# Kernel optimization log

Hardware: AMD Instinct MI355X
Metric: run time of the kernel (lower is better)

The kernel has to match this reference:

```python
import jax, jax.numpy as jnp
import numpy as np

BN_EPS = 1e-5
LEAKY_SLOPE = 0.01
DK = 64


def setup_inputs() -> dict:
    key = jax.random.key(0)
    ks = jax.random.split(key, 9)
    B, N, C = 8, 2048, 256
    H, dk, dv = 8, 64, 64
    return {
        "x": jax.random.normal(ks[0], (B, N, C), jnp.float32),
        "Wq": jax.random.normal(ks[1], (H, dk, C), jnp.float32) * (1.0 / np.sqrt(C)),
        "Wk": jax.random.normal(ks[2], (H, dk, C), jnp.float32) * (1.0 / np.sqrt(C)),
        "Wv": jax.random.normal(ks[3], (H, dv, C), jnp.float32) * (1.0 / np.sqrt(C)),
        "Wp": jax.random.normal(ks[4], (C, H * dv), jnp.float32) * (1.0 / np.sqrt(H * dv)),
        "bn_gamma": jax.random.uniform(ks[5], (C,), jnp.float32, 0.5, 1.5),
        "bn_beta": jax.random.normal(ks[6], (C,), jnp.float32) * 0.1,
        "bn_mean": jax.random.normal(ks[7], (C,), jnp.float32) * 0.1,
        "bn_var": jax.random.uniform(ks[8], (C,), jnp.float32, 0.5, 1.5),
    }


def reference(x, Wq, Wk, Wv, Wp, bn_gamma, bn_beta, bn_mean, bn_var):
    # x: [B,N,C]; per-head 1x1 Conv1d projections batched over heads h.
    q = jnp.einsum("bnc,hkc->bhnk", x, Wq)   # [B,H,N,dk]
    k = jnp.einsum("bnc,hkc->bhnk", x, Wk)   # [B,H,N,dk]
    v = jnp.einsum("bnc,hvc->bhnv", x, Wv)   # [B,H,N,dv]
    energy = jnp.einsum("bhnk,bhmk->bhnm", q, k)  # [B,H,N,N]
    scale = 1.0 / jnp.sqrt(jnp.float32(DK))
    attn = jax.nn.softmax(energy * scale, axis=-1)
    xw = jnp.einsum("bhnm,bhmv->bhnv", attn, v)   # [B,H,N,dv]
    # torch.cat(heads, dim=2) -> [B,N,H*dv] with head-major ordering
    B, H, N, dv = xw.shape
    cat = jnp.transpose(xw, (0, 2, 1, 3)).reshape(B, N, H * dv)
    # LBRD: 1x1 conv (no bias) + BatchNorm1d (inference stats) + LeakyReLU + Dropout(0)
    y = jnp.einsum("bnf,cf->bnc", cat, Wp)
    y = (y - bn_mean) * (bn_gamma * jax.lax.rsqrt(bn_var + BN_EPS)) + bn_beta
    y = jnp.where(y >= 0, y, LEAKY_SLOPE * y)
    return y
```

## Files before the change

kernel.cpp:

```cpp
#include <hip/hip_runtime.h>
#include <hip/hip_bf16.h>

typedef unsigned short u16;
typedef unsigned int u32;
typedef float  f32x4 __attribute__((ext_vector_type(4)));
typedef short  s16x8 __attribute__((ext_vector_type(8)));

#define DEV static __device__ __forceinline__

DEV u16 f2bf(float f){ union{float f; unsigned int i;} c; c.f=f; unsigned int i=c.i;
                       return (u16)((i + 0x7FFFu + ((i>>16)&1u))>>16); }

DEV u32 pkbf(float a, float b){
  union{ __hip_bfloat162 h; u32 u; } c;
  c.h = __float22bfloat162_rn(make_float2(a, b));
  return c.u;
}

DEV float exp2a(float x){
#if __has_builtin(__builtin_amdgcn_exp2f)
  return __builtin_amdgcn_exp2f(x);
#else
  return exp2f(x);
#endif
}

DEV s16x8 ld_frag(const u16* p){
  union{ s16x8 v; uint2 u[2]; } r;
  r.u[0] = *(const uint2*)(p);
  r.u[1] = *(const uint2*)(p+16);
  return r.v;
}

__global__ __launch_bounds__(256) void cvt_kernel(const float* __restrict__ src,
                                                  u16* __restrict__ dst, int n4)
{
  int i = blockIdx.x*256 + threadIdx.x;
  if (i >= n4) return;
  float4 v = *(const float4*)(src + (size_t)i*4);
  ushort4 o;
  o.x = f2bf(v.x); o.y = f2bf(v.y); o.z = f2bf(v.z); o.w = f2bf(v.w);
  *(ushort4*)(dst + (size_t)i*4) = o;
}

__global__ __launch_bounds__(256) void kv_kernel(
    const u16* __restrict__ x, const u16* __restrict__ Wk,
    const u16* __restrict__ Wv, u16* __restrict__ kbuf, u16* __restrict__ vbuf)
{
  const int isV = blockIdx.z;
  const u16* W = isV ? Wv : Wk;
  const int m0 = blockIdx.x*64, j0 = blockIdx.y*64;
  __shared__ u16 at[64][40];
  __shared__ u16 bt[64][40];
  const int tid = threadIdx.x, lane = tid&63, w = tid>>6;
  const int wm = w>>1, wn = w&1;
  const int l16 = lane&15, lq = lane>>4;
  f32x4 acc[2][2] = {};
  const int srow = tid>>2, scol = (tid&3)*8;
  for (int c0=0;c0<256;c0+=32){
    *(uint4*)&at[srow][scol] = *(const uint4*)&x[(size_t)(m0+srow)*256 + c0 + scol];
    *(uint4*)&bt[srow][scol] = *(const uint4*)&W[(size_t)(j0+srow)*256 + c0 + scol];
    __syncthreads();
    s16x8 af[2], bfr[2];
    #pragma unroll
    for(int mf=0;mf<2;mf++) af[mf]  = ld_frag(&at[wm*32+mf*16+l16][lq*4]);
    #pragma unroll
    for(int nf=0;nf<2;nf++) bfr[nf] = ld_frag(&bt[wn*32+nf*16+l16][lq*4]);
    #pragma unroll
    for(int mf=0;mf<2;mf++)
      #pragma unroll
      for(int nf=0;nf<2;nf++)
        acc[mf][nf] = __builtin_amdgcn_mfma_f32_16x16x32_bf16(af[mf], bfr[nf], acc[mf][nf],0,0,0);
    __syncthreads();
  }
  if (!isV){
    #pragma unroll
    for(int mf=0;mf<2;mf++)
      #pragma unroll
      for(int nf=0;nf<2;nf++){
        const int j  = j0 + wn*32 + nf*16 + l16;
        const int hh = j>>6;
        const int kkp = wn*32 + (l16>>2)*8 + nf*4 + (l16&3);
        #pragma unroll
        for(int r=0;r<4;r++){
          int m = m0 + wm*32 + mf*16 + lq*4 + r;
          int blx = m>>11, n = m&2047;
          kbuf[(size_t)((blx<<3)|hh)*131072 + (size_t)n*64 + kkp] = f2bf(acc[mf][nf][r]);
        }
      }
  } else {
    const int blx = m0>>11;
    #pragma unroll
    for(int mf=0;mf<2;mf++){
      const int nn = (m0&2047) + wm*32 + lq*8 + mf*4;
      #pragma unroll
      for(int nf=0;nf<2;nf++){
        const int j  = j0 + wn*32 + nf*16 + l16;
        const int hh = j>>6, kk = j&63;
        uint2 st;
        st.x = pkbf(acc[mf][nf][0], acc[mf][nf][1]);
        st.y = pkbf(acc[mf][nf][2], acc[mf][nf][3]);
        *(uint2*)&vbuf[(size_t)((blx<<3)|hh)*131072 + (size_t)kk*2048 + nn] = st;
      }
    }
  }
}

__global__ __launch_bounds__(256) void attn_kernel(
    const u16* __restrict__ x, const u16* __restrict__ Wq,
    const u16* __restrict__ kb, const u16* __restrict__ vb,
    u16* __restrict__ cat, int bh_per_xcd)
{
  const int lin = blockIdx.x;
  const int xcd = lin & 7, slot = lin >> 3;
  const int bhl = xcd*bh_per_xcd + (slot>>4);
  const int n0  = (slot & 15) * 128;
  const int bl = bhl>>3, h = bhl&7;
  const u16* xg = x + (size_t)bl*524288;
  const u16* kg = kb + (size_t)bhl*131072;
  const u16* vg = vb + (size_t)bhl*131072;
  u16* catp = cat + (size_t)bl*1048576 + h*64;
  const int tid=threadIdx.x, lane=tid&63, w=tid>>6;
  const int l16=lane&15, lq=lane>>4;

  __shared__ __align__(16) u16 kt[64][72];
  __shared__ __align__(16) u16 vt[64][72];

  s16x8 qf[2][2];
  {
    const u16* wqh = Wq + (size_t)h*16384;
    s16x8 xf[2][8];
    #pragma unroll
    for(int sub=0;sub<2;sub++){
      const int row = n0 + w*32 + sub*16 + l16;
      #pragma unroll
      for(int kc8=0;kc8<8;kc8++) xf[sub][kc8] = ld_frag(xg + (size_t)row*256 + kc8*32 + lq*4);
    }
    f32x4 dq[2][4] = {};
    #pragma unroll
    for(int df=0;df<4;df++)
      #pragma unroll
      for(int kc8=0;kc8<8;kc8++){
        s16x8 wf = ld_frag(wqh + (size_t)(df*16+l16)*256 + kc8*32 + lq*4);
        dq[0][df] = __builtin_amdgcn_mfma_f32_16x16x32_bf16(wf, xf[0][kc8], dq[0][df],0,0,0);
        dq[1][df] = __builtin_amdgcn_mfma_f32_16x16x32_bf16(wf, xf[1][kc8], dq[1][df],0,0,0);
      }
    const float SCL = 0.125f * 1.44269504088896f;
    #pragma unroll
    for(int sub=0;sub<2;sub++)
      #pragma unroll
      for(int kc=0;kc<2;kc++){
        union{s16x8 v; u32 u[4];} t;
        t.u[0]=pkbf(dq[sub][2*kc][0]*SCL,  dq[sub][2*kc][1]*SCL);
        t.u[1]=pkbf(dq[sub][2*kc][2]*SCL,  dq[sub][2*kc][3]*SCL);
        t.u[2]=pkbf(dq[sub][2*kc+1][0]*SCL,dq[sub][2*kc+1][1]*SCL);
        t.u[3]=pkbf(dq[sub][2*kc+1][2]*SCL,dq[sub][2*kc+1][3]*SCL);
        qf[sub][kc]=t.v;
      }
  }

  s16x8 ones;
  #pragma unroll
  for(int e=0;e<8;e++) ones[e] = (short)0x3F80;

  const int srow = tid>>2, sc = (tid&3)*16;
  const u16* kst = kg + (size_t)srow*64 + sc;
  const u16* vst = vg + (size_t)srow*2048 + sc;
  uint4 kr0,kr1,vr0,vr1;
  kr0 = *(const uint4*)(kst);   kr1 = *(const uint4*)(kst+8);
  vr0 = *(const uint4*)(vst);   vr1 = *(const uint4*)(vst+8);
  *(uint4*)&kt[srow][sc] = kr0;  *(uint4*)&kt[srow][sc+8] = kr1;
  *(uint4*)&vt[srow][sc] = vr0;  *(uint4*)&vt[srow][sc+8] = vr1;
  kr0 = *(const uint4*)(kst + 4096);  kr1 = *(const uint4*)(kst + 4096 + 8);
  vr0 = *(const uint4*)(vst + 64);    vr1 = *(const uint4*)(vst + 64 + 8);
  __syncthreads();

  f32x4 oacc[2][4] = {};
  f32x4 accl[2] = {};

  for(int t=0;t<32;t++){
    s16x8 kf[8], vf[8];
    #pragma unroll
    for(int jf=0;jf<4;jf++)
      #pragma unroll
      for(int kc=0;kc<2;kc++)
        kf[jf*2+kc] = *(const s16x8*)&kt[jf*16+l16][kc*32+lq*8];
    #pragma unroll
    for(int cf=0;cf<4;cf++)
      #pragma unroll
      for(int kc=0;kc<2;kc++)
        vf[cf*2+kc] = *(const s16x8*)&vt[cf*16+l16][kc*32+lq*8];

    if (t<31){
      __syncthreads();
      *(uint4*)&kt[srow][sc]   = kr0;  *(uint4*)&kt[srow][sc+8] = kr1;
      *(uint4*)&vt[srow][sc]   = vr0;  *(uint4*)&vt[srow][sc+8] = vr1;
      if (t<30){
        kr0 = *(const uint4*)(kst + (size_t)(t+2)*4096);
        kr1 = *(const uint4*)(kst + (size_t)(t+2)*4096 + 8);
        vr0 = *(const uint4*)(vst + (size_t)(t+2)*64);
        vr1 = *(const uint4*)(vst + (size_t)(t+2)*64 + 8);
      }
    }

    f32x4 sacc[2][4] = {};
    #pragma unroll
    for(int jf=0;jf<4;jf++)
      #pragma unroll
      for(int kc=0;kc<2;kc++){
        sacc[0][jf]=__builtin_amdgcn_mfma_f32_16x16x32_bf16(kf[jf*2+kc],qf[0][kc],sacc[0][jf],0,0,0);
        sacc[1][jf]=__builtin_amdgcn_mfma_f32_16x16x32_bf16(kf[jf*2+kc],qf[1][kc],sacc[1][jf],0,0,0);
      }
    s16x8 pf[2][2];
    #pragma unroll
    for(int sub=0;sub<2;sub++)
      #pragma unroll
      for(int kc=0;kc<2;kc++){
        union{s16x8 v; u32 u[4];} tt;
        tt.u[0]=pkbf(exp2a(sacc[sub][2*kc][0]),  exp2a(sacc[sub][2*kc][1]));
        tt.u[1]=pkbf(exp2a(sacc[sub][2*kc][2]),  exp2a(sacc[sub][2*kc][3]));
        tt.u[2]=pkbf(exp2a(sacc[sub][2*kc+1][0]),exp2a(sacc[sub][2*kc+1][1]));
        tt.u[3]=pkbf(exp2a(sacc[sub][2*kc+1][2]),exp2a(sacc[sub][2*kc+1][3]));
        pf[sub][kc]=tt.v;
      }
    #pragma unroll
    for(int kc=0;kc<2;kc++){
      accl[0]=__builtin_amdgcn_mfma_f32_16x16x32_bf16(ones,pf[0][kc],accl[0],0,0,0);
      accl[1]=__builtin_amdgcn_mfma_f32_16x16x32_bf16(ones,pf[1][kc],accl[1],0,0,0);
    }
    #pragma unroll
    for(int cf=0;cf<4;cf++)
      #pragma unroll
      for(int kc=0;kc<2;kc++){
        oacc[0][cf]=__builtin_amdgcn_mfma_f32_16x16x32_bf16(vf[cf*2+kc],pf[0][kc],oacc[0][cf],0,0,0);
        oacc[1][cf]=__builtin_amdgcn_mfma_f32_16x16x32_bf16(vf[cf*2+kc],pf[1][kc],oacc[1][cf],0,0,0);
      }
    if (t<31) __syncthreads();
  }
  #pragma unroll
  for(int sub=0;sub<2;sub++){
    const float rinv = 1.f/accl[sub][0];
    const int n = n0 + w*32 + sub*16 + l16;
    #pragma unroll
    for(int cf=0;cf<4;cf++){
      uint2 st;
      st.x = pkbf(oacc[sub][cf][0]*rinv, oacc[sub][cf][1]*rinv);
      st.y = pkbf(oacc[sub][cf][2]*rinv, oacc[sub][cf][3]*rinv);
      *(uint2*)(catp + (size_t)n*512 + cf*16 + lq*4) = st;
    }
  }
}

__global__ __launch_bounds__(256) void proj_kernel(
    const u16* __restrict__ cat, const u16* __restrict__ Wp,
    const float* __restrict__ gamma, const float* __restrict__ beta,
    const float* __restrict__ mean,  const float* __restrict__ var,
    float* __restrict__ out)
{
  const int m0 = blockIdx.x*64, j0 = blockIdx.y*64;
  __shared__ u16 at[64][40];
  __shared__ u16 bt[64][40];
  const int tid=threadIdx.x, lane=tid&63, w=tid>>6;
  const int wm=w>>1, wn=w&1, l16=lane&15, lq=lane>>4;
  f32x4 acc[2][2]={};
  const int srow=tid>>2, scol=(tid&3)*8;
  for(int c0=0;c0<512;c0+=32){
    *(uint4*)&at[srow][scol] = *(const uint4*)&cat[(size_t)(m0+srow)*512 + c0+scol];
    *(uint4*)&bt[srow][scol] = *(const uint4*)&Wp[(size_t)(j0+srow)*512 + c0+scol];
    __syncthreads();
    s16x8 af[2],bfr[2];
    #pragma unroll
    for(int mf=0;mf<2;mf++) af[mf]=ld_frag(&at[wm*32+mf*16+l16][lq*4]);
    #pragma unroll
    for(int nf=0;nf<2;nf++) bfr[nf]=ld_frag(&bt[wn*32+nf*16+l16][lq*4]);
    #pragma unroll
    for(int mf=0;mf<2;mf++)
      #pragma unroll
      for(int nf=0;nf<2;nf++)
        acc[mf][nf]=__builtin_amdgcn_mfma_f32_16x16x32_bf16(af[mf],bfr[nf],acc[mf][nf],0,0,0);
    __syncthreads();
  }
  #pragma unroll
  for(int nf=0;nf<2;nf++){
    const int co = j0 + wn*32 + nf*16 + l16;
    const float g=gamma[co], be=beta[co], mu=mean[co], va=var[co];
    const float a  = g * rsqrtf(va + 1e-5f);
    const float b2 = be - mu*a;
    #pragma unroll
    for(int mf=0;mf<2;mf++)
      #pragma unroll
      for(int r=0;r<4;r++){
        int m = m0 + wm*32 + mf*16 + lq*4 + r;
        float y = acc[mf][nf][r]*a + b2;
        y = (y>=0.f)? y : 0.01f*y;
        out[(size_t)m*256 + co] = y;
      }
  }
}

extern "C" void kernel_launch(void* const* d_in, const int* in_sizes, int n_in,
                              void* d_out, int out_size, void* d_ws, size_t ws_size,
                              hipStream_t stream)
{
  const float* x  = (const float*)d_in[0];
  const float* Wq = (const float*)d_in[1];
  const float* Wk = (const float*)d_in[2];
  const float* Wv = (const float*)d_in[3];
  const float* Wp = (const float*)d_in[4];
  const float* g  = (const float*)d_in[5];
  const float* be = (const float*)d_in[6];
  const float* mu = (const float*)d_in[7];
  const float* va = (const float*)d_in[8];

  u16* ws   = (u16*)d_ws;
  u16* x16  = ws;
  u16* wq16 = ws + 4194304;
  u16* wk16 = ws + 4325376;
  u16* wv16 = ws + 4456448;
  u16* wp16 = ws + 4587520;
  u16* kb   = ws + 4718592;

  cvt_kernel<<<4096, 256, 0, stream>>>(x,  x16,  1048576);
  cvt_kernel<<<128,  256, 0, stream>>>(Wq, wq16, 32768);
  cvt_kernel<<<128,  256, 0, stream>>>(Wk, wk16, 32768);
  cvt_kernel<<<128,  256, 0, stream>>>(Wv, wv16, 32768);
  cvt_kernel<<<128,  256, 0, stream>>>(Wp, wp16, 32768);

  const size_t full_elems = 4718592ull + 8388608ull*3ull;
  if (ws_size >= full_elems*2ull){
    u16* vb  = kb + 8388608;
    u16* cat = vb + 8388608;
    kv_kernel<<<dim3(256,8,2), dim3(256), 0, stream>>>(x16, wk16, wv16, kb, vb);
    attn_kernel<<<dim3(1024), dim3(256), 0, stream>>>(x16, wq16, kb, vb, cat, 8);
    proj_kernel<<<dim3(256,4), dim3(256), 0, stream>>>(cat, wp16, g, be, mu, va, (float*)d_out);
  } else {
    u16* vb  = kb + 4194304;
    u16* cat = vb + 4194304;
    for (int half = 0; half < 2; ++half){
      const u16* xh = x16 + (size_t)half*2097152;
      u16* cath = cat + (size_t)half*4194304;
      kv_kernel<<<dim3(128,8,2), dim3(256), 0, stream>>>(xh, wk16, wv16, kb, vb);
      attn_kernel<<<dim3(512), dim3(256), 0, stream>>>(xh, wq16, kb, vb, cath, 4);
    }
    proj_kernel<<<dim3(256,4), dim3(256), 0, stream>>>(cat, wp16, g, be, mu, va, (float*)d_out);
  }
}
```

Before: 177.4 us.

## Load K/V fragments directly from global memory, dropping LDS staging and barriers

The attention kernel no longer stages K and V tiles through shared memory with register prefetch and block barriers. Each wave now reads its MFMA fragments straight from global memory (relying on L1/L2), and the launch bounds request 3 blocks per CU for occupancy. This removes the LDS writes and reads plus two __syncthreads per iteration. In exchange, each of the four waves fetches the same K/V data redundantly from cache, and the loads are no longer prefetched ahead of use, so memory latency may be exposed.

```diff
diff --git a/kernel.cpp b/kernel.cpp
--- a/kernel.cpp
+++ b/kernel.cpp
@@ -106,7 +106,7 @@
   }
 }
 
-__global__ __launch_bounds__(256) void attn_kernel(
+__global__ __launch_bounds__(256,3) void attn_kernel(
     const u16* __restrict__ x, const u16* __restrict__ Wq,
     const u16* __restrict__ kb, const u16* __restrict__ vb,
     u16* __restrict__ cat, int bh_per_xcd)
@@ -123,9 +123,6 @@
   const int tid=threadIdx.x, lane=tid&63, w=tid>>6;
   const int l16=lane&15, lq=lane>>4;
 
-  __shared__ __align__(16) u16 kt[64][72];
-  __shared__ __align__(16) u16 vt[64][72];
-
   s16x8 qf[2][2];
   {
     const u16* wqh = Wq + (size_t)h*16384;
@@ -163,17 +160,8 @@
   #pragma unroll
   for(int e=0;e<8;e++) ones[e] = (short)0x3F80;
 
-  const int srow = tid>>2, sc = (tid&3)*16;
-  const u16* kst = kg + (size_t)srow*64 + sc;
-  const u16* vst = vg + (size_t)srow*2048 + sc;
-  uint4 kr0,kr1,vr0,vr1;
-  kr0 = *(const uint4*)(kst);   kr1 = *(const uint4*)(kst+8);
-  vr0 = *(const uint4*)(vst);   vr1 = *(const uint4*)(vst+8);
-  *(uint4*)&kt[srow][sc] = kr0;  *(uint4*)&kt[srow][sc+8] = kr1;
-  *(uint4*)&vt[srow][sc] = vr0;  *(uint4*)&vt[srow][sc+8] = vr1;
-  kr0 = *(const uint4*)(kst + 4096);  kr1 = *(const uint4*)(kst + 4096 + 8);
-  vr0 = *(const uint4*)(vst + 64);    vr1 = *(const uint4*)(vst + 64 + 8);
-  __syncthreads();
+  const u16* kfb = kg + (size_t)l16*64 + lq*8;
+  const u16* vfb = vg + (size_t)l16*2048 + lq*8;
 
   f32x4 oacc[2][4] = {};
   f32x4 accl[2] = {};
@@ -184,24 +172,12 @@
     for(int jf=0;jf<4;jf++)
       #pragma unroll
       for(int kc=0;kc<2;kc++)
-        kf[jf*2+kc] = *(const s16x8*)&kt[jf*16+l16][kc*32+lq*8];
+        kf[jf*2+kc] = *(const s16x8*)(kfb + (size_t)t*4096 + jf*1024 + kc*32);
     #pragma unroll
     for(int cf=0;cf<4;cf++)
       #pragma unroll
       for(int kc=0;kc<2;kc++)
-        vf[cf*2+kc] = *(const s16x8*)&vt[cf*16+l16][kc*32+lq*8];
-
-    if (t<31){
-      __syncthreads();
-      *(uint4*)&kt[srow][sc]   = kr0;  *(uint4*)&kt[srow][sc+8] = kr1;
-      *(uint4*)&vt[srow][sc]   = vr0;  *(uint4*)&vt[srow][sc+8] = vr1;
-      if (t<30){
-        kr0 = *(const uint4*)(kst + (size_t)(t+2)*4096);
-        kr1 = *(const uint4*)(kst + (size_t)(t+2)*4096 + 8);
-        vr0 = *(const uint4*)(vst + (size_t)(t+2)*64);
-        vr1 = *(const uint4*)(vst + (size_t)(t+2)*64 + 8);
-      }
-    }
+        vf[cf*2+kc] = *(const s16x8*)(vfb + (size_t)cf*32768 + (size_t)t*64 + kc*32);
 
     f32x4 sacc[2][4] = {};
     #pragma unroll
@@ -235,7 +211,6 @@
         oacc[0][cf]=__builtin_amdgcn_mfma_f32_16x16x32_bf16(vf[cf*2+kc],pf[0][kc],oacc[0][cf],0,0,0);
         oacc[1][cf]=__builtin_amdgcn_mfma_f32_16x16x32_bf16(vf[cf*2+kc],pf[1][kc],oacc[1][cf],0,0,0);
       }
-    if (t<31) __syncthreads();
   }
   #pragma unroll
   for(int sub=0;sub<2;sub++){
```

Result: slower. 328.5 us (+85.2%).

## Fuse fp32-to-bf16 conversion of x into KV and attention loads

Applied to the files above, without the earlier changes.

Drops the standalone conversion pass over x and has kv_kernel and attn_kernel read fp32 x directly, packing it to bf16 in registers as they load. The four weight conversions are merged into one launch using a 2D grid. This removes a full read and write of x plus four kernel launches, but x is now read at twice the bytes by the consumers, and the KV kernel reads it from both its K and V blocks.

```diff
diff --git a/kernel.cpp b/kernel.cpp
--- a/kernel.cpp
+++ b/kernel.cpp
@@ -32,11 +32,26 @@
   return r.v;
 }
 
-__global__ __launch_bounds__(256) void cvt_kernel(const float* __restrict__ src,
-                                                  u16* __restrict__ dst, int n4)
-{
+DEV s16x8 ld_frag_f32(const float* p){
+  float4 a = *(const float4*)(p);
+  float4 b = *(const float4*)(p+16);
+  union{ s16x8 v; u32 u[4]; } r;
+  r.u[0]=pkbf(a.x,a.y); r.u[1]=pkbf(a.z,a.w);
+  r.u[2]=pkbf(b.x,b.y); r.u[3]=pkbf(b.z,b.w);
+  return r.v;
+}
+
+__global__ __launch_bounds__(256) void cvt_w_kernel(
+    const float* __restrict__ w0, const float* __restrict__ w1,
+    const float* __restrict__ w2, const float* __restrict__ w3,
+    u16* __restrict__ d0, u16* __restrict__ d1,
+    u16* __restrict__ d2, u16* __restrict__ d3)
+{
+  const int z = blockIdx.y;
+  const float* src = (z==0)?w0:(z==1)?w1:(z==2)?w2:w3;
+  u16* dst = (z==0)?d0:(z==1)?d1:(z==2)?d2:d3;
   int i = blockIdx.x*256 + threadIdx.x;
-  if (i >= n4) return;
+  if (i >= 32768) return;
   float4 v = *(const float4*)(src + (size_t)i*4);
   ushort4 o;
   o.x = f2bf(v.x); o.y = f2bf(v.y); o.z = f2bf(v.z); o.w = f2bf(v.w);
@@ -44,7 +59,7 @@
 }
 
 __global__ __launch_bounds__(256) void kv_kernel(
-    const u16* __restrict__ x, const u16* __restrict__ Wk,
+    const float* __restrict__ x32, const u16* __restrict__ Wk,
     const u16* __restrict__ Wv, u16* __restrict__ kbuf, u16* __restrict__ vbuf)
 {
   const int isV = blockIdx.z;
@@ -58,7 +73,13 @@
   f32x4 acc[2][2] = {};
   const int srow = tid>>2, scol = (tid&3)*8;
   for (int c0=0;c0<256;c0+=32){
-    *(uint4*)&at[srow][scol] = *(const uint4*)&x[(size_t)(m0+srow)*256 + c0 + scol];
+    {
+      const float* xs = x32 + (size_t)(m0+srow)*256 + c0 + scol;
+      float4 a = *(const float4*)xs;
+      float4 b = *(const float4*)(xs+4);
+      uint4 st; st.x=pkbf(a.x,a.y); st.y=pkbf(a.z,a.w); st.z=pkbf(b.x,b.y); st.w=pkbf(b.z,b.w);
+      *(uint4*)&at[srow][scol] = st;
+    }
     *(uint4*)&bt[srow][scol] = *(const uint4*)&W[(size_t)(j0+srow)*256 + c0 + scol];
     __syncthreads();
     s16x8 af[2], bfr[2];
@@ -107,7 +128,7 @@
 }
 
 __global__ __launch_bounds__(256) void attn_kernel(
-    const u16* __restrict__ x, const u16* __restrict__ Wq,
+    const float* __restrict__ x32, const u16* __restrict__ Wq,
     const u16* __restrict__ kb, const u16* __restrict__ vb,
     u16* __restrict__ cat, int bh_per_xcd)
 {
@@ -116,7 +137,7 @@
   const int bhl = xcd*bh_per_xcd + (slot>>4);
   const int n0  = (slot & 15) * 128;
   const int bl = bhl>>3, h = bhl&7;
-  const u16* xg = x + (size_t)bl*524288;
+  const float* xg = x32 + (size_t)bl*524288;
   const u16* kg = kb + (size_t)bhl*131072;
   const u16* vg = vb + (size_t)bhl*131072;
   u16* catp = cat + (size_t)bl*1048576 + h*64;
@@ -134,7 +155,8 @@
     for(int sub=0;sub<2;sub++){
       const int row = n0 + w*32 + sub*16 + l16;
       #pragma unroll
-      for(int kc8=0;kc8<8;kc8++) xf[sub][kc8] = ld_frag(xg + (size_t)row*256 + kc8*32 + lq*4);
+      for(int kc8=0;kc8<8;kc8++)
+        xf[sub][kc8] = ld_frag_f32(xg + (size_t)row*256 + kc8*32 + lq*4);
     }
     f32x4 dq[2][4] = {};
     #pragma unroll
@@ -313,31 +335,26 @@
   const float* va = (const float*)d_in[8];
 
   u16* ws   = (u16*)d_ws;
-  u16* x16  = ws;
-  u16* wq16 = ws + 4194304;
-  u16* wk16 = ws + 4325376;
-  u16* wv16 = ws + 4456448;
-  u16* wp16 = ws + 4587520;
-  u16* kb   = ws + 4718592;
-
-  cvt_kernel<<<4096, 256, 0, stream>>>(x,  x16,  1048576);
-  cvt_kernel<<<128,  256, 0, stream>>>(Wq, wq16, 32768);
-  cvt_kernel<<<128,  256, 0, stream>>>(Wk, wk16, 32768);
-  cvt_kernel<<<128,  256, 0, stream>>>(Wv, wv16, 32768);
-  cvt_kernel<<<128,  256, 0, stream>>>(Wp, wp16, 32768);
-
-  const size_t full_elems = 4718592ull + 8388608ull*3ull;
+  u16* wq16 = ws;
+  u16* wk16 = ws + 131072;
+  u16* wv16 = ws + 262144;
+  u16* wp16 = ws + 393216;
+  u16* kb   = ws + 524288;
+
+  cvt_w_kernel<<<dim3(128,4), 256, 0, stream>>>(Wq, Wk, Wv, Wp, wq16, wk16, wv16, wp16);
+
+  const size_t full_elems = 524288ull + 8388608ull*3ull;
   if (ws_size >= full_elems*2ull){
     u16* vb  = kb + 8388608;
     u16* cat = vb + 8388608;
-    kv_kernel<<<dim3(256,8,2), dim3(256), 0, stream>>>(x16, wk16, wv16, kb, vb);
-    attn_kernel<<<dim3(1024), dim3(256), 0, stream>>>(x16, wq16, kb, vb, cat, 8);
+    kv_kernel<<<dim3(256,8,2), dim3(256), 0, stream>>>(x, wk16, wv16, kb, vb);
+    attn_kernel<<<dim3(1024), dim3(256), 0, stream>>>(x, wq16, kb, vb, cat, 8);
     proj_kernel<<<dim3(256,4), dim3(256), 0, stream>>>(cat, wp16, g, be, mu, va, (float*)d_out);
   } else {
     u16* vb  = kb + 4194304;
     u16* cat = vb + 4194304;
     for (int half = 0; half < 2; ++half){
-      const u16* xh = x16 + (size_t)half*2097152;
+      const float* xh = x + (size_t)half*2097152;
       u16* cath = cat + (size_t)half*4194304;
       kv_kernel<<<dim3(128,8,2), dim3(256), 0, stream>>>(xh, wk16, wv16, kb, vb);
       attn_kernel<<<dim3(512), dim3(256), 0, stream>>>(xh, wq16, kb, vb, cath, 4);
```

After: 172.0 us. -3.1%, faster.
